# Kernel tuning notes

Measured on AMD Instinct MI355X. Metric: run time of the kernel, lower is better.

The kernel has to match this reference:

```python
import jax, jax.numpy as jnp
import numpy as np

NUM_HEADS = 16
ROPE_THETA = 10000.0
RMS_EPS = 1e-6


def _rope(t):
    # t: [B, L, H, D]; standard interleaved rotary embedding over sequence positions
    B, L, H, D = t.shape
    half = D // 2
    inv_freq = 1.0 / (ROPE_THETA ** (jnp.arange(half, dtype=jnp.float32) / half))
    ang = jnp.arange(L, dtype=jnp.float32)[:, None] * inv_freq[None, :]  # [L, half]
    cos = jnp.cos(ang)[None, :, None, :]  # [1, L, 1, half]
    sin = jnp.sin(ang)[None, :, None, :]
    t1 = t[..., 0::2]
    t2 = t[..., 1::2]
    r1 = t1 * cos - t2 * sin
    r2 = t1 * sin + t2 * cos
    out = jnp.stack([r1, r2], axis=-1).reshape(B, L, H, D)
    return out


def _qk_rms_norm(t, gamma):
    # t: [B, L, H, D]; gamma: [H, D] learned scale per head-channel
    rms = jnp.sqrt(jnp.mean(jnp.square(t), axis=-1, keepdims=True) + RMS_EPS)
    return (t / rms) * gamma[None, None, :, :]


def setup_inputs() -> dict:
    key = jax.random.key(0)
    ks = jax.random.split(key, 5)
    B, L, C = 2, 2048, 1024
    x = jax.random.normal(ks[0], (B, L, C), dtype=jnp.float32)
    w_qkv = jax.random.normal(ks[1], (3 * C, C), dtype=jnp.float32) * 0.02
    b_qkv = jax.random.normal(ks[2], (3 * C,), dtype=jnp.float32) * 0.02
    w_out = jax.random.normal(ks[3], (C, C), dtype=jnp.float32) * 0.02
    b_out = jax.random.normal(ks[4], (C,), dtype=jnp.float32) * 0.02
    q_gamma = jnp.ones((NUM_HEADS, C // NUM_HEADS), dtype=jnp.float32)
    k_gamma = jnp.ones((NUM_HEADS, C // NUM_HEADS), dtype=jnp.float32)
    return {"x": x, "w_qkv": w_qkv, "b_qkv": b_qkv, "w_out": w_out,
            "b_out": b_out, "q_gamma": q_gamma, "k_gamma": k_gamma}


def reference(x, w_qkv, b_qkv, w_out, b_out, q_gamma, k_gamma):
    B, L, C = x.shape
    H = NUM_HEADS
    D = C // H
    # fused QKV projection -> [B, L, 3, H, D]
    qkv = (x @ w_qkv.T + b_qkv).reshape(B, L, 3, H, D)
    q, k, v = qkv[:, :, 0], qkv[:, :, 1], qkv[:, :, 2]  # each [B, L, H, D]
    # inline RoPE on q, k
    q = _rope(q)
    k = _rope(k)
    # QK RMSNorm with learned per-head scale
    q = _qk_rms_norm(q, q_gamma)
    k = _qk_rms_norm(k, k_gamma)
    # full (non-causal) scaled dot-product attention
    scale = 1.0 / jnp.sqrt(jnp.float32(D))
    scores = jnp.einsum('blhd,bmhd->bhlm', q, k) * scale  # [B, H, L, L]
    attn = jax.nn.softmax(scores, axis=-1)
    o = jnp.einsum('bhlm,bmhd->blhd', attn, v).reshape(B, L, C)
    return o @ w_out.T + b_out
```

## Files before the change

### kernel.cpp

```cpp
#include <hip/hip_runtime.h>
#include <stdint.h>

typedef __attribute__((ext_vector_type(8))) short short8;
typedef __attribute__((ext_vector_type(4))) float f32x4;
typedef __attribute__((ext_vector_type(16))) float f32x16;

#define LOG2E 1.44269504088896f

__device__ __forceinline__ float bf2f(uint16_t u) {
    union { uint32_t i; float f; } v; v.i = ((uint32_t)u) << 16; return v.f;
}
__device__ __forceinline__ uint16_t f2bf(float f) {
    union { float f; uint32_t i; } v; v.f = f;
    return (uint16_t)((v.i + 0x7fffu + ((v.i >> 16) & 1u)) >> 16);
}

__global__ void cast3_kernel(const float4* __restrict__ a, int na,
                             const float4* __restrict__ b, int nb,
                             const float4* __restrict__ c, int nc,
                             uint64_t* __restrict__ oa, uint64_t* __restrict__ ob,
                             uint64_t* __restrict__ oc) {
    int stride = gridDim.x * blockDim.x;
    int ntot = na + nb + nc;
    for (int i = blockIdx.x * blockDim.x + threadIdx.x; i < ntot; i += stride) {
        const float4* src; uint64_t* dst; int j;
        if (i < na)           { src = a; dst = oa; j = i; }
        else if (i < na + nb) { src = b; dst = ob; j = i - na; }
        else                  { src = c; dst = oc; j = i - na - nb; }
        float4 v = src[j];
        dst[j] = (uint64_t)f2bf(v.x) | ((uint64_t)f2bf(v.y) << 16)
               | ((uint64_t)f2bf(v.z) << 32) | ((uint64_t)f2bf(v.w) << 48);
    }
}

__global__ void rope_table_kernel(float2* __restrict__ tab) {
    int idx = blockIdx.x * 256 + threadIdx.x;
    int l = idx >> 5, i = idx & 31;
    float fr = powf(10000.0f, -(float)i * (1.0f / 32.0f));
    float ang = (float)l * fr;
    float s, c;
    sincosf(ang, &s, &c);
    tab[idx] = make_float2(c, s);
}

template<bool OUTBF>
__global__ __launch_bounds__(256, 2) void gemm_bt(
    const uint16_t* __restrict__ A, const uint16_t* __restrict__ Bw,
    const float* __restrict__ bias, void* __restrict__ outp,
    int M, int N, int K)
{
    __shared__ uint16_t Asm[128 * 64];
    __shared__ uint16_t Bsm[128 * 64];
    int tid = threadIdx.x;
    int wave = tid >> 6, lane = tid & 63;
    int bm = blockIdx.y * 128, bn = blockIdx.x * 128;
    int wm = (wave >> 1) * 64, wn = (wave & 1) * 64;

    f32x4 acc[4][4] = {};

    int srow = lane >> 3;
    int sc16 = lane & 7;

    for (int k0 = 0; k0 < K; k0 += 64) {
#pragma unroll
        for (int c = 0; c < 4; ++c) {
            int chunk = wave * 4 + c;
            int row = chunk * 8 + srow;
            int col = ((sc16 ^ (row & 7)) << 3);
            __builtin_amdgcn_global_load_lds(
                (const __attribute__((address_space(1))) void*)(A + (size_t)(bm + row) * K + k0 + col),
                (__attribute__((address_space(3))) void*)(Asm + chunk * 512),
                16, 0, 0);
            __builtin_amdgcn_global_load_lds(
                (const __attribute__((address_space(1))) void*)(Bw + (size_t)(bn + row) * K + k0 + col),
                (__attribute__((address_space(3))) void*)(Bsm + chunk * 512),
                16, 0, 0);
        }
        __syncthreads();
#pragma unroll
        for (int kk = 0; kk < 2; ++kk) {
            short8 af[4], bfr[4];
#pragma unroll
            for (int m = 0; m < 4; ++m) {
                int row = wm + m * 16 + (lane & 15);
                int kc = kk * 4 + (lane >> 4);
                af[m] = *(const short8*)(Asm + row * 64 + ((kc ^ (row & 7)) << 3));
            }
#pragma unroll
            for (int n = 0; n < 4; ++n) {
                int row = wn + n * 16 + (lane & 15);
                int kc = kk * 4 + (lane >> 4);
                bfr[n] = *(const short8*)(Bsm + row * 64 + ((kc ^ (row & 7)) << 3));
            }
#pragma unroll
            for (int m = 0; m < 4; ++m)
#pragma unroll
                for (int n = 0; n < 4; ++n)
                    acc[m][n] = __builtin_amdgcn_mfma_f32_16x16x32_bf16(af[m], bfr[n], acc[m][n], 0, 0, 0);
        }
        __syncthreads();
    }
#pragma unroll
    for (int m = 0; m < 4; ++m) {
#pragma unroll
        for (int n = 0; n < 4; ++n) {
            int col = bn + wn + n * 16 + (lane & 15);
            float bv = bias[col];
#pragma unroll
            for (int r = 0; r < 4; ++r) {
                int row = bm + wm + m * 16 + (lane >> 4) * 4 + r;
                float val = acc[m][n][r] + bv;
                if (OUTBF) ((uint16_t*)outp)[(size_t)row * N + col] = f2bf(val);
                else       ((float*)outp)[(size_t)row * N + col] = val;
            }
        }
    }
}

__global__ void rope_rms_kernel(const uint16_t* __restrict__ qkv, const float2* __restrict__ tab,
                                const float* __restrict__ qg, const float* __restrict__ kg,
                                uint16_t* __restrict__ Q, uint16_t* __restrict__ Kk, uint16_t* __restrict__ V)
{
    int bl = blockIdx.x;
    int h = blockIdx.y * 4 + (threadIdx.x >> 6);
    int d = threadIdx.x & 63;
    int l = bl & 2047;
    const uint16_t* base = qkv + (size_t)bl * 3072 + h * 64;
    size_t outoff = ((((size_t)(bl >> 11)) * 16 + h) * 2048 + l) * 64 + d;

    V[outoff] = base[2048 + d];

    float2 cs = tab[l * 32 + (d >> 1)];
    float sg = (d & 1) ? cs.y : -cs.y;
    {
        float t = bf2f(base[d]);
        float p = bf2f(base[d ^ 1]);
        float r = t * cs.x + p * sg;
        float ss = r * r;
#pragma unroll
        for (int m = 32; m >= 1; m >>= 1) ss += __shfl_xor(ss, m);
        float scale = rsqrtf(ss * (1.0f / 64.0f) + 1e-6f) * qg[h * 64 + d] * (0.125f * LOG2E);
        Q[outoff] = f2bf(r * scale);
    }
    {
        float t = bf2f(base[1024 + d]);
        float p = bf2f(base[1024 + (d ^ 1)]);
        float r = t * cs.x + p * sg;
        float ss = r * r;
#pragma unroll
        for (int m = 32; m >= 1; m >>= 1) ss += __shfl_xor(ss, m);
        float scale = rsqrtf(ss * (1.0f / 64.0f) + 1e-6f) * kg[h * 64 + d];
        Kk[outoff] = f2bf(r * scale);
    }
}

__global__ __launch_bounds__(256, 2) void flash_kernel(
    const uint16_t* __restrict__ Q, const uint16_t* __restrict__ K, const uint16_t* __restrict__ V,
    uint16_t* __restrict__ O)
{
    __shared__ __align__(16) uint16_t lds[16384];
    uint16_t* Ksm = lds;
    uint16_t* Vsm = lds + 8192;

    int tid = threadIdx.x, wave = tid >> 6, lane = tid & 63;
    int lq = lane & 31;
    int hi = lane >> 5;
    int bh = blockIdx.y;
    int q0 = blockIdx.x * 128 + wave * 32;
    const uint16_t* Qb = Q + (size_t)bh * 2048 * 64;
    const uint16_t* Kb = K + (size_t)bh * 2048 * 64;
    const uint16_t* Vb = V + (size_t)bh * 2048 * 64;

    short8 qf[4];
#pragma unroll
    for (int kb = 0; kb < 4; ++kb)
        qf[kb] = *(const short8*)(Qb + (size_t)(q0 + lq) * 64 + kb * 16 + hi * 8);

    f32x16 oacc0 = {}, oacc1 = {};
    float lsum = 0.0f;

    int kvp = tid & 31, dg = tid >> 5;
    int r8 = lane >> 3, sl = lane & 7;
    int srccol = (sl ^ r8) << 3;

#pragma unroll
    for (int c = 0; c < 2; ++c) {
        int ch = wave * 2 + c;
        __builtin_amdgcn_global_load_lds(
            (const __attribute__((address_space(1))) void*)(Kb + (size_t)(ch * 8 + r8) * 64 + srccol),
            (__attribute__((address_space(3))) void*)(Ksm + ch * 512), 16, 0, 0);
    }
    short8 va  = *(const short8*)(Vb + (size_t)(kvp * 2) * 64 + dg * 8);
    short8 vb2 = *(const short8*)(Vb + (size_t)(kvp * 2 + 1) * 64 + dg * 8);

    int buf = 0;
    for (int t = 0; t < 32; ++t) {
        {
            char* Vbase = (char*)(Vsm + buf * 4096);
#pragma unroll
            for (int j = 0; j < 8; ++j) {
                uint32_t wd = (uint32_t)(uint16_t)va[j] | ((uint32_t)(uint16_t)vb2[j] << 16);
                *(uint32_t*)(Vbase + (dg * 8 + j) * 128 + (((kvp >> 2) ^ j) << 4) + ((kvp & 3) << 2)) = wd;
            }
        }
        __syncthreads();

        if (t < 31) {
            int kv0n = (t + 1) * 64;
#pragma unroll
            for (int c = 0; c < 2; ++c) {
                int ch = wave * 2 + c;
                __builtin_amdgcn_global_load_lds(
                    (const __attribute__((address_space(1))) void*)(Kb + (size_t)(kv0n + ch * 8 + r8) * 64 + srccol),
                    (__attribute__((address_space(3))) void*)(Ksm + (buf ^ 1) * 4096 + ch * 512), 16, 0, 0);
            }
            va  = *(const short8*)(Vb + (size_t)(kv0n + kvp * 2) * 64 + dg * 8);
            vb2 = *(const short8*)(Vb + (size_t)(kv0n + kvp * 2 + 1) * 64 + dg * 8);
        }

        const uint16_t* Kbase = Ksm + buf * 4096;
        f32x16 st0 = {}, st1 = {};
        __builtin_amdgcn_s_setprio(1);
#pragma unroll
        for (int kb = 0; kb < 4; ++kb) {
            int sw = ((hi + 2 * kb) ^ (lq & 7)) << 3;
            short8 kf0 = *(const short8*)(Kbase + lq * 64 + sw);
            short8 kf1 = *(const short8*)(Kbase + (32 + lq) * 64 + sw);
            st0 = __builtin_amdgcn_mfma_f32_32x32x16_bf16(kf0, qf[kb], st0, 0, 0, 0);
            st1 = __builtin_amdgcn_mfma_f32_32x32x16_bf16(kf1, qf[kb], st1, 0, 0, 0);
        }
        __builtin_amdgcn_s_setprio(0);

        float rs0 = 0.0f, rs1 = 0.0f;
        uint32_t w0[4][2], w1[4][2];
#pragma unroll
        for (int qd = 0; qd < 4; ++qd) {
#pragma unroll
            for (int k2 = 0; k2 < 2; ++k2) {
                float a0 = exp2f(st0[qd * 4 + k2 * 2]);
                float a1 = exp2f(st0[qd * 4 + k2 * 2 + 1]);
                rs0 += a0 + a1;
                asm("v_cvt_pk_bf16_f32 %0, %1, %2" : "=v"(w0[qd][k2]) : "v"(a0), "v"(a1));
                float b0 = exp2f(st1[qd * 4 + k2 * 2]);
                float b1 = exp2f(st1[qd * 4 + k2 * 2 + 1]);
                rs1 += b0 + b1;
                asm("v_cvt_pk_bf16_f32 %0, %1, %2" : "=v"(w1[qd][k2]) : "v"(b0), "v"(b1));
            }
        }
        lsum += rs0 + rs1;

        __builtin_amdgcn_s_setprio(1);
#pragma unroll
        for (int c = 0; c < 4; ++c) {
            int s = c & 1;
            uint32_t A0, B0, A1, B1;
            if (c < 2) { A0 = w0[s * 2][0]; B0 = w0[s * 2 + 1][0]; A1 = w0[s * 2][1]; B1 = w0[s * 2 + 1][1]; }
            else       { A0 = w1[s * 2][0]; B0 = w1[s * 2 + 1][0]; A1 = w1[s * 2][1]; B1 = w1[s * 2 + 1][1]; }
            asm volatile("v_permlane32_swap_b32 %0, %1" : "+v"(A0), "+v"(B0));
            asm volatile("v_permlane32_swap_b32 %0, %1" : "+v"(A1), "+v"(B1));
            union { uint32_t u[4]; short8 s8; } pu;
            pu.u[0] = A0; pu.u[1] = A1; pu.u[2] = B0; pu.u[3] = B1;
            int sw = ((2 * c + hi) ^ (lq & 7)) << 3;
            const uint16_t* Vbase = Vsm + buf * 4096;
            short8 vf0 = *(const short8*)(Vbase + lq * 64 + sw);
            short8 vf1 = *(const short8*)(Vbase + (32 + lq) * 64 + sw);
            oacc0 = __builtin_amdgcn_mfma_f32_32x32x16_bf16(vf0, pu.s8, oacc0, 0, 0, 0);
            oacc1 = __builtin_amdgcn_mfma_f32_32x32x16_bf16(vf1, pu.s8, oacc1, 0, 0, 0);
        }
        __builtin_amdgcn_s_setprio(0);
        buf ^= 1;
    }

    lsum += __shfl_xor(lsum, 32);
    __syncthreads();
    float inv = 1.0f / lsum;
    char* Osm = (char*)(lds + wave * 2304);
#pragma unroll
    for (int qd = 0; qd < 4; ++qd) {
#pragma unroll
        for (int k2 = 0; k2 < 2; ++k2) {
            int dbase = 8 * qd + 4 * hi + 2 * k2;
            float p0 = oacc0[qd * 4 + k2 * 2] * inv, p1 = oacc0[qd * 4 + k2 * 2 + 1] * inv;
            uint32_t wd;
            asm("v_cvt_pk_bf16_f32 %0, %1, %2" : "=v"(wd) : "v"(p0), "v"(p1));
            *(uint32_t*)(Osm + lq * 144 + dbase * 2) = wd;
            float p2 = oacc1[qd * 4 + k2 * 2] * inv, p3 = oacc1[qd * 4 + k2 * 2 + 1] * inv;
            asm("v_cvt_pk_bf16_f32 %0, %1, %2" : "=v"(wd) : "v"(p2), "v"(p3));
            *(uint32_t*)(Osm + lq * 144 + (32 + dbase) * 2) = wd;
        }
    }
    asm volatile("s_waitcnt lgkmcnt(0)" ::: "memory");
    int q2 = lane >> 1, hf = lane & 1;
    char* OsmR = (char*)(lds + wave * 2304);
    size_t orow = (size_t)((bh >> 4) * 2048 + blockIdx.x * 128 + wave * 32 + q2) * 1024
                + (size_t)(bh & 15) * 64 + hf * 32;
#pragma unroll
    for (int ch = 0; ch < 4; ++ch) {
        short8 o = *(const short8*)(OsmR + q2 * 144 + hf * 64 + ch * 16);
        *(short8*)(O + orow + ch * 8) = o;
    }
}

extern "C" void kernel_launch(void* const* d_in, const int* in_sizes, int n_in,
                              void* d_out, int out_size, void* d_ws, size_t ws_size,
                              hipStream_t stream)
{
    const float* x      = (const float*)d_in[0];
    const float* w_qkv  = (const float*)d_in[1];
    const float* b_qkv  = (const float*)d_in[2];
    const float* w_out  = (const float*)d_in[3];
    const float* b_out  = (const float*)d_in[4];
    const float* qg     = (const float*)d_in[5];
    const float* kg     = (const float*)d_in[6];
    float* out = (float*)d_out;

    char* w = (char*)d_ws;
    uint16_t* x_bf    = (uint16_t*)w;  w += (size_t)4096 * 1024 * 2;
    uint16_t* wqkv_bf = (uint16_t*)w;  w += (size_t)3072 * 1024 * 2;
    uint16_t* wout_bf = (uint16_t*)w;  w += (size_t)1024 * 1024 * 2;
    float2*   tab     = (float2*)w;    w += (size_t)2048 * 32 * 8;
    uint16_t* qkv_bf  = (uint16_t*)w;  w += (size_t)4096 * 3072 * 2;
    uint16_t* Qb      = (uint16_t*)w;  w += (size_t)4096 * 1024 * 2;
    uint16_t* Kb      = (uint16_t*)w;  w += (size_t)4096 * 1024 * 2;
    uint16_t* Vb      = (uint16_t*)w;  w += (size_t)4096 * 1024 * 2;
    uint16_t* attn_bf = (uint16_t*)w;  w += (size_t)4096 * 1024 * 2;

    cast3_kernel<<<2048, 256, 0, stream>>>(
        (const float4*)x, 4096 * 1024 / 4,
        (const float4*)w_qkv, 3072 * 1024 / 4,
        (const float4*)w_out, 1024 * 1024 / 4,
        (uint64_t*)x_bf, (uint64_t*)wqkv_bf, (uint64_t*)wout_bf);
    rope_table_kernel<<<256, 256, 0, stream>>>(tab);

    gemm_bt<true><<<dim3(24, 32), 256, 0, stream>>>(x_bf, wqkv_bf, b_qkv, qkv_bf, 4096, 3072, 1024);
    rope_rms_kernel<<<dim3(4096, 4), 256, 0, stream>>>(qkv_bf, tab, qg, kg, Qb, Kb, Vb);
    flash_kernel<<<dim3(16, 32), 256, 0, stream>>>(Qb, Kb, Vb, attn_bf);
    gemm_bt<false><<<dim3(8, 32), 256, 0, stream>>>(attn_bf, wout_bf, b_out, out, 4096, 1024, 1024);
}
```

Measured before the change: 219.1 us.

## Split KV range across two wave groups in flash kernel and merge via LDS

The attention kernel now runs 512 threads per block. Two groups of four waves each handle half of the key/value sequence for the same 128 query rows, and their output accumulators and row sums are then combined through shared memory. Since the softmax keeps no running max, the partial results can simply be added. The aim is more waves per CU and a shorter serial KV loop per block. The price is a larger LDS footprint (64 KB per block), an extra reduction step, and register pressure under the tighter launch bounds, which could spill. Separately, the fused three-tensor cast kernel is split back into three launches.

Result: slower. 232.7 us (+6.2%).

```diff
diff --git a/kernel.cpp b/kernel.cpp
--- a/kernel.cpp
+++ b/kernel.cpp
@@ -15,21 +15,13 @@
     return (uint16_t)((v.i + 0x7fffu + ((v.i >> 16) & 1u)) >> 16);
 }
 
-__global__ void cast3_kernel(const float4* __restrict__ a, int na,
-                             const float4* __restrict__ b, int nb,
-                             const float4* __restrict__ c, int nc,
-                             uint64_t* __restrict__ oa, uint64_t* __restrict__ ob,
-                             uint64_t* __restrict__ oc) {
+__global__ void cast_kernel(const float4* __restrict__ in, uint64_t* __restrict__ out, int n4) {
     int stride = gridDim.x * blockDim.x;
-    int ntot = na + nb + nc;
-    for (int i = blockIdx.x * blockDim.x + threadIdx.x; i < ntot; i += stride) {
-        const float4* src; uint64_t* dst; int j;
-        if (i < na)           { src = a; dst = oa; j = i; }
-        else if (i < na + nb) { src = b; dst = ob; j = i - na; }
-        else                  { src = c; dst = oc; j = i - na - nb; }
-        float4 v = src[j];
-        dst[j] = (uint64_t)f2bf(v.x) | ((uint64_t)f2bf(v.y) << 16)
-               | ((uint64_t)f2bf(v.z) << 32) | ((uint64_t)f2bf(v.w) << 48);
+    for (int i = blockIdx.x * blockDim.x + threadIdx.x; i < n4; i += stride) {
+        float4 v = in[i];
+        uint64_t o = (uint64_t)f2bf(v.x) | ((uint64_t)f2bf(v.y) << 16)
+                   | ((uint64_t)f2bf(v.z) << 32) | ((uint64_t)f2bf(v.w) << 48);
+        out[i] = o;
     }
 }
 
@@ -154,19 +146,21 @@
     }
 }
 
-__global__ __launch_bounds__(256, 2) void flash_kernel(
+__global__ __launch_bounds__(512, 4) void flash_kernel(
     const uint16_t* __restrict__ Q, const uint16_t* __restrict__ K, const uint16_t* __restrict__ V,
     uint16_t* __restrict__ O)
 {
-    __shared__ __align__(16) uint16_t lds[16384];
-    uint16_t* Ksm = lds;
-    uint16_t* Vsm = lds + 8192;
-
+    __shared__ __align__(16) uint16_t lds[32768];
     int tid = threadIdx.x, wave = tid >> 6, lane = tid & 63;
+    int qw = wave & 3, half = wave >> 2;
+    uint16_t* Ksm = lds + half * 16384;
+    uint16_t* Vsm = Ksm + 8192;
+
     int lq = lane & 31;
     int hi = lane >> 5;
     int bh = blockIdx.y;
-    int q0 = blockIdx.x * 128 + wave * 32;
+    int q0 = blockIdx.x * 128 + qw * 32;
+    int kvbase = half * 1024;
     const uint16_t* Qb = Q + (size_t)bh * 2048 * 64;
     const uint16_t* Kb = K + (size_t)bh * 2048 * 64;
     const uint16_t* Vb = V + (size_t)bh * 2048 * 64;
@@ -179,22 +173,23 @@
     f32x16 oacc0 = {}, oacc1 = {};
     float lsum = 0.0f;
 
-    int kvp = tid & 31, dg = tid >> 5;
+    int tid_h = tid & 255;
+    int kvp = tid_h & 31, dg = tid_h >> 5;
     int r8 = lane >> 3, sl = lane & 7;
     int srccol = (sl ^ r8) << 3;
 
 #pragma unroll
     for (int c = 0; c < 2; ++c) {
-        int ch = wave * 2 + c;
+        int ch = qw * 2 + c;
         __builtin_amdgcn_global_load_lds(
-            (const __attribute__((address_space(1))) void*)(Kb + (size_t)(ch * 8 + r8) * 64 + srccol),
+            (const __attribute__((address_space(1))) void*)(Kb + (size_t)(kvbase + ch * 8 + r8) * 64 + srccol),
             (__attribute__((address_space(3))) void*)(Ksm + ch * 512), 16, 0, 0);
     }
-    short8 va  = *(const short8*)(Vb + (size_t)(kvp * 2) * 64 + dg * 8);
-    short8 vb2 = *(const short8*)(Vb + (size_t)(kvp * 2 + 1) * 64 + dg * 8);
+    short8 va  = *(const short8*)(Vb + (size_t)(kvbase + kvp * 2) * 64 + dg * 8);
+    short8 vb2 = *(const short8*)(Vb + (size_t)(kvbase + kvp * 2 + 1) * 64 + dg * 8);
 
     int buf = 0;
-    for (int t = 0; t < 32; ++t) {
+    for (int t = 0; t < 16; ++t) {
         {
             char* Vbase = (char*)(Vsm + buf * 4096);
 #pragma unroll
@@ -205,11 +200,11 @@
         }
         __syncthreads();
 
-        if (t < 31) {
-            int kv0n = (t + 1) * 64;
+        if (t < 15) {
+            int kv0n = kvbase + (t + 1) * 64;
 #pragma unroll
             for (int c = 0; c < 2; ++c) {
-                int ch = wave * 2 + c;
+                int ch = qw * 2 + c;
                 __builtin_amdgcn_global_load_lds(
                     (const __attribute__((address_space(1))) void*)(Kb + (size_t)(kv0n + ch * 8 + r8) * 64 + srccol),
                     (__attribute__((address_space(3))) void*)(Ksm + (buf ^ 1) * 4096 + ch * 512), 16, 0, 0);
@@ -273,8 +268,28 @@
 
     lsum += __shfl_xor(lsum, 32);
     __syncthreads();
+    float* cb = (float*)lds;
+    if (half == 1) {
+        int b0 = qw * 33 * 64;
+#pragma unroll
+        for (int i = 0; i < 16; ++i) cb[b0 + i * 64 + lane] = oacc0[i];
+#pragma unroll
+        for (int i = 0; i < 16; ++i) cb[b0 + (16 + i) * 64 + lane] = oacc1[i];
+        cb[b0 + 32 * 64 + lane] = lsum;
+    }
+    __syncthreads();
+    if (half == 1) return;
+    {
+        int b0 = qw * 33 * 64;
+#pragma unroll
+        for (int i = 0; i < 16; ++i) oacc0[i] += cb[b0 + i * 64 + lane];
+#pragma unroll
+        for (int i = 0; i < 16; ++i) oacc1[i] += cb[b0 + (16 + i) * 64 + lane];
+        lsum += cb[b0 + 32 * 64 + lane];
+    }
+
     float inv = 1.0f / lsum;
-    char* Osm = (char*)(lds + wave * 2304);
+    char* Osm = (char*)(lds + 18432) + qw * 4608;
 #pragma unroll
     for (int qd = 0; qd < 4; ++qd) {
 #pragma unroll
@@ -291,12 +306,11 @@
     }
     asm volatile("s_waitcnt lgkmcnt(0)" ::: "memory");
     int q2 = lane >> 1, hf = lane & 1;
-    char* OsmR = (char*)(lds + wave * 2304);
-    size_t orow = (size_t)((bh >> 4) * 2048 + blockIdx.x * 128 + wave * 32 + q2) * 1024
+    size_t orow = (size_t)((bh >> 4) * 2048 + blockIdx.x * 128 + qw * 32 + q2) * 1024
                 + (size_t)(bh & 15) * 64 + hf * 32;
 #pragma unroll
     for (int ch = 0; ch < 4; ++ch) {
-        short8 o = *(const short8*)(OsmR + q2 * 144 + hf * 64 + ch * 16);
+        short8 o = *(const short8*)(Osm + q2 * 144 + hf * 64 + ch * 16);
         *(short8*)(O + orow + ch * 8) = o;
     }
 }
@@ -325,15 +339,13 @@
     uint16_t* Vb      = (uint16_t*)w;  w += (size_t)4096 * 1024 * 2;
     uint16_t* attn_bf = (uint16_t*)w;  w += (size_t)4096 * 1024 * 2;
 
-    cast3_kernel<<<2048, 256, 0, stream>>>(
-        (const float4*)x, 4096 * 1024 / 4,
-        (const float4*)w_qkv, 3072 * 1024 / 4,
-        (const float4*)w_out, 1024 * 1024 / 4,
-        (uint64_t*)x_bf, (uint64_t*)wqkv_bf, (uint64_t*)wout_bf);
+    cast_kernel<<<2048, 256, 0, stream>>>((const float4*)x,     (uint64_t*)x_bf,    4096 * 1024 / 4);
+    cast_kernel<<<2048, 256, 0, stream>>>((const float4*)w_qkv, (uint64_t*)wqkv_bf, 3072 * 1024 / 4);
+    cast_kernel<<<1024, 256, 0, stream>>>((const float4*)w_out, (uint64_t*)wout_bf, 1024 * 1024 / 4);
     rope_table_kernel<<<256, 256, 0, stream>>>(tab);
 
     gemm_bt<true><<<dim3(24, 32), 256, 0, stream>>>(x_bf, wqkv_bf, b_qkv, qkv_bf, 4096, 3072, 1024);
     rope_rms_kernel<<<dim3(4096, 4), 256, 0, stream>>>(qkv_bf, tab, qg, kg, Qb, Kb, Vb);
-    flash_kernel<<<dim3(16, 32), 256, 0, stream>>>(Qb, Kb, Vb, attn_bf);
+    flash_kernel<<<dim3(16, 32), 512, 0, stream>>>(Qb, Kb, Vb, attn_bf);
     gemm_bt<false><<<dim3(8, 32), 256, 0, stream>>>(attn_bf, wout_bf, b_out, out, 4096, 1024, 1024);
 }
```
